# Kernel tuning notes

Measured on AMD Instinct MI355X. Metric: run time of the kernel, lower is better.

The kernel has to match this reference:

```python
import jax, jax.numpy as jnp
import numpy as np

S, H, R, Z, P = 268, 1024, 8, 8, 4
A = S - Z - P          # actual_hidden_dim = 256
E = min(Z, P)          # min_embed_dim = 4
B = 8192


def setup_inputs() -> dict:
    key = jax.random.key(0)
    ks = jax.random.split(key, 16)
    def g(k, shape, scale=0.02):
        return jax.random.normal(k, shape, dtype=jnp.float32) * scale
    return dict(
        t=jax.random.uniform(ks[0], (1,), dtype=jnp.float32) * 24.0,
        state=jax.random.normal(ks[1], (B, S), dtype=jnp.float32),
        W0=g(ks[2], (H, S + 2)), b0=jnp.zeros((H,), jnp.float32),
        res_W1=g(ks[3], (R, H, H)), res_b1=jnp.zeros((R, H), jnp.float32),
        res_W2=g(ks[4], (R, H, H)), res_b2=jnp.zeros((R, H), jnp.float32),
        Wf=g(ks[5], (S, H)), bf=jnp.zeros((S,), jnp.float32),
        lp_in_w=g(ks[6], (3 * E, E)), lp_in_b=jnp.zeros((3 * E,), jnp.float32),
        lp_out_w=g(ks[7], (E, E)), lp_out_b=jnp.zeros((E,), jnp.float32),
        ta_in_w=g(ks[8], (3 * A, A)), ta_in_b=jnp.zeros((3 * A,), jnp.float32),
        ta_out_w=g(ks[9], (A, A)), ta_out_b=jnp.zeros((A,), jnp.float32),
        loc_proj_w=g(ks[10], (E, Z)), loc_proj_b=jnp.zeros((E,), jnp.float32),
        loc_back_w=g(ks[11], (Z, E)), loc_back_b=jnp.zeros((Z,), jnp.float32),
    )


def reference(t, state, W0, b0, res_W1, res_b1, res_W2, res_b2, Wf, bf,
              lp_in_w, lp_in_b, lp_out_w, lp_out_b,
              ta_in_w, ta_in_b, ta_out_w, ta_out_b,
              loc_proj_w, loc_proj_b, loc_back_w, loc_back_b):
    Bn = state.shape[0]
    # time features: [sin(2*pi*t/24), cos(2*pi*t/24)] broadcast to [B, 2]
    ang = t * (2.0 * jnp.pi / 24.0)
    t_vec = jnp.broadcast_to(jnp.concatenate([jnp.sin(ang), jnp.cos(ang)]), (Bn, 2))

    # core MLP trunk: Linear -> ReLU -> R residual blocks -> Linear
    x = jnp.concatenate([state, t_vec], axis=-1)
    h = jax.nn.relu(x @ W0.T + b0)

    def block(h, p):
        W1, b1, W2, b2 = p
        return jnp.tanh(h + jnp.tanh(h @ W1.T + b1) @ W2.T + b2), None

    h, _ = jax.lax.scan(block, h, (res_W1, res_b1, res_W2, res_b2))
    core = h @ Wf.T + bf  # [B, S]

    # Attention deltas. Both MHA calls have key/value seq_len == 1, so the
    # softmax over a single key is exactly 1.0 and the output reduces exactly
    # to out_proj(v_proj(value)); Q/K projections (and the padded time query)
    # cancel mathematically. Same math as nn.MultiheadAttention here.
    h_part = state[:, :A]
    loc = state[:, A:A + Z]
    loc_p = loc @ loc_proj_w.T + loc_proj_b                   # [B, E]
    v = loc_p @ lp_in_w[2 * E:].T + lp_in_b[2 * E:]           # V projection
    enhanced_loc = v @ lp_out_w.T + lp_out_b                  # out projection
    delta_loc = (enhanced_loc - loc_p) @ loc_back_w.T + loc_back_b  # [B, Z]

    v2 = h_part @ ta_in_w[2 * A:].T + ta_in_b[2 * A:]
    enhanced_h = v2 @ ta_out_w.T + ta_out_b
    delta_h = enhanced_h - h_part                             # [B, A]

    delta = jnp.concatenate(
        [delta_h, delta_loc, jnp.zeros((Bn, P), state.dtype)], axis=-1)
    return core + 0.1 * delta
```

## Files before the change

kernel.cpp:

```cpp
#include <hip/hip_runtime.h>
#include <hip/hip_bf16.h>


typedef unsigned short u16;
typedef __bf16 bf16x8 __attribute__((ext_vector_type(8)));
typedef float f32x4 __attribute__((ext_vector_type(4)));

__device__ __forceinline__ u16 f2b(float f) {
  union { float f; unsigned u; } v; v.f = f;
  unsigned r = v.u + 0x7FFFu + ((v.u >> 16) & 1u);
  return (u16)(r >> 16);
}
__device__ __forceinline__ float b2f(u16 s) {
  union { unsigned u; float f; } v; v.u = ((unsigned)s) << 16;
  return v.f;
}

__device__ __forceinline__ void g2l16(const u16* g, u16* l) {
  __builtin_amdgcn_global_load_lds(
      (__attribute__((address_space(1))) void*)g,
      (__attribute__((address_space(3))) void*)l, 16, 0, 0);
}

template<int MODE, int KK, int LDA>
__global__ __launch_bounds__(512, 4)
void pgemm(const u16* __restrict__ A, const u16* __restrict__ W,
           const float* __restrict__ bias, const u16* __restrict__ resid,
           void* __restrict__ outp, int nreal, int ldo)
{
  extern __shared__ __align__(16) u16 sm[];
  constexpr int BUFSZ = (128 + 128) * 64;

  const int tid  = threadIdx.x;
  const int wave = tid >> 6;
  const int lane = tid & 63;
  const int m0 = blockIdx.x << 7;
  const int n0 = blockIdx.y << 7;
  const int wr = wave >> 2, wc = wave & 3;
  const int lrow = lane & 15, quad = lane >> 4;
  const int sw = lrow & 7;

  const int srow  = lane >> 3;
  const int sperm = ((lane & 7) ^ (srow & 7)) << 3;

  const u16* Ag = A + (size_t)(m0 + wave * 16 + srow) * LDA + sperm;
  const u16* Bg = W + (size_t)(n0 + wave * 16 + srow) * KK + sperm;

  f32x4 acc[4][2];
#pragma unroll
  for (int i = 0; i < 4; i++)
#pragma unroll
    for (int j = 0; j < 2; j++) { f32x4 z = {0.f,0.f,0.f,0.f}; acc[i][j] = z; }

  auto stage = [&](int p, int buf) {
    const int ko = p << 6;
    u16* aD = sm + buf * BUFSZ;
    u16* bD = aD + 128 * 64;
    g2l16(Ag + ko,                        aD + (wave * 16 + 0) * 64);
    g2l16(Ag + (size_t)8 * LDA + ko,      aD + (wave * 16 + 8) * 64);
    g2l16(Bg + ko,                        bD + (wave * 16 + 0) * 64);
    g2l16(Bg + (size_t)8 * KK + ko,       bD + (wave * 16 + 8) * 64);
  };

  constexpr int P = KK / 64;

  stage(0, 0);

  for (int p = 0; p < P; ++p) {
    if (p + 1 < P) {
      stage(p + 1, (p + 1) & 1);
      asm volatile("s_waitcnt vmcnt(4)" ::: "memory");
    } else {
      asm volatile("s_waitcnt vmcnt(0)" ::: "memory");
    }
    __builtin_amdgcn_sched_barrier(0);
    __builtin_amdgcn_s_barrier();
    __builtin_amdgcn_sched_barrier(0);

    const u16* aS = sm + (p & 1) * BUFSZ;
    const u16* bS = aS + 128 * 64;
#pragma unroll
    for (int s = 0; s < 2; s++) {
      const int phys = (s * 4 + quad) ^ sw;
      bf16x8 af[4], bfr[2];
#pragma unroll
      for (int i = 0; i < 4; i++)
        af[i] = *(const bf16x8*)&aS[(wr * 64 + i * 16 + lrow) * 64 + phys * 8];
#pragma unroll
      for (int j = 0; j < 2; j++)
        bfr[j] = *(const bf16x8*)&bS[(wc * 32 + j * 16 + lrow) * 64 + phys * 8];
      __builtin_amdgcn_s_setprio(1);
#pragma unroll
      for (int i = 0; i < 4; i++)
#pragma unroll
        for (int j = 0; j < 2; j++)
          acc[i][j] = __builtin_amdgcn_mfma_f32_16x16x32_bf16(af[i], bfr[j], acc[i][j], 0, 0, 0);
      __builtin_amdgcn_s_setprio(0);
    }
    __builtin_amdgcn_sched_barrier(0);
    __builtin_amdgcn_s_barrier();
    __builtin_amdgcn_sched_barrier(0);
  }

  auto th = [](float x) {
    x = fminf(fmaxf(x, -40.f), 40.f);
    float a = __builtin_amdgcn_exp2f(2.88539008177793f * x);
    return (a - 1.f) * __builtin_amdgcn_rcpf(a + 1.f);
  };

#pragma unroll
  for (int i = 0; i < 4; i++) {
    const int rowb = m0 + wr * 64 + i * 16 + quad * 4;
#pragma unroll
    for (int j = 0; j < 2; j++) {
      const int col = n0 + wc * 32 + j * 16 + lrow;
      const float bi = (col < nreal) ? bias[col] : 0.f;
#pragma unroll
      for (int r = 0; r < 4; r++) {
        const int row = rowb + r;
        float v = acc[i][j][r] + bi;
        if (MODE == 0) {
          v = v > 0.f ? v : 0.f;
          ((u16*)outp)[(size_t)row * ldo + col] = f2b(v);
        } else if (MODE == 1) {
          ((u16*)outp)[(size_t)row * ldo + col] = f2b(th(v));
        } else if (MODE == 2) {
          v += b2f(resid[(size_t)row * ldo + col]);
          ((u16*)outp)[(size_t)row * ldo + col] = f2b(th(v));
        } else if (MODE == 3) {
          if (col < nreal) ((float*)outp)[(size_t)row * ldo + col] = v;
        }
      }
    }
  }
}

__global__ __launch_bounds__(256, 4)
void gemm_bt(const u16* __restrict__ A, const u16* __restrict__ B,
             const float* __restrict__ bias, u16* __restrict__ outp,
             int K, int lda, int ldo)
{
  __shared__ __align__(16) u16 As[64 * 64];
  __shared__ __align__(16) u16 Bs[128 * 64];
  const int tid  = threadIdx.x;
  const int wave = tid >> 6;
  const int lane = tid & 63;
  const int m0 = blockIdx.y << 6;
  const int n0 = blockIdx.x << 7;
  const int wr = wave >> 1, wc = wave & 1;
  const int lrow = lane & 15, quad = lane >> 4;
  const int srow  = lane >> 3;
  const int sperm = ((lane & 7) ^ (srow & 7)) << 3;

  const u16* Ag0 = A + (size_t)(m0 + wave * 16 +  0 + srow) * lda + sperm;
  const u16* Ag1 = A + (size_t)(m0 + wave * 16 +  8 + srow) * lda + sperm;
  const u16* Bg0 = B + (size_t)(n0 + wave * 32 +  0 + srow) * K + sperm;
  const u16* Bg1 = B + (size_t)(n0 + wave * 32 +  8 + srow) * K + sperm;
  const u16* Bg2 = B + (size_t)(n0 + wave * 32 + 16 + srow) * K + sperm;
  const u16* Bg3 = B + (size_t)(n0 + wave * 32 + 24 + srow) * K + sperm;
  u16* Al0 = &As[(wave * 16 +  0) * 64];
  u16* Al1 = &As[(wave * 16 +  8) * 64];
  u16* Bl0 = &Bs[(wave * 32 +  0) * 64];
  u16* Bl1 = &Bs[(wave * 32 +  8) * 64];
  u16* Bl2 = &Bs[(wave * 32 + 16) * 64];
  u16* Bl3 = &Bs[(wave * 32 + 24) * 64];

  f32x4 acc[2][4];
#pragma unroll
  for (int i = 0; i < 2; i++)
#pragma unroll
    for (int j = 0; j < 4; j++) { f32x4 z = {0.f,0.f,0.f,0.f}; acc[i][j] = z; }

  const int swz = lrow & 7;

  for (int k0 = 0; k0 < K; k0 += 64) {
    if (k0) __syncthreads();
    g2l16(Ag0 + k0, Al0);
    g2l16(Ag1 + k0, Al1);
    g2l16(Bg0 + k0, Bl0);
    g2l16(Bg1 + k0, Bl1);
    g2l16(Bg2 + k0, Bl2);
    g2l16(Bg3 + k0, Bl3);
    __syncthreads();
#pragma unroll
    for (int s = 0; s < 2; s++) {
      const int c = (s * 4 + quad) ^ swz;
      bf16x8 af[2], bfr[4];
#pragma unroll
      for (int i = 0; i < 2; i++)
        af[i] = *(const bf16x8*)&As[(wr * 32 + i * 16 + lrow) * 64 + c * 8];
#pragma unroll
      for (int j = 0; j < 4; j++)
        bfr[j] = *(const bf16x8*)&Bs[(wc * 64 + j * 16 + lrow) * 64 + c * 8];
#pragma unroll
      for (int i = 0; i < 2; i++)
#pragma unroll
        for (int j = 0; j < 4; j++)
          acc[i][j] = __builtin_amdgcn_mfma_f32_16x16x32_bf16(af[i], bfr[j], acc[i][j], 0, 0, 0);
    }
  }

#pragma unroll
  for (int i = 0; i < 2; i++) {
    const int rowb = m0 + wr * 32 + i * 16 + quad * 4;
#pragma unroll
    for (int j = 0; j < 4; j++) {
      const int col = n0 + wc * 64 + j * 16 + lrow;
      const float bi = bias[col];
#pragma unroll
      for (int r = 0; r < 4; r++)
        outp[(size_t)(rowb + r) * ldo + col] = f2b(acc[i][j][r] + bi);
    }
  }
}

__global__ void conv_bulk(const float* __restrict__ w1, const float* __restrict__ w2,
                          u16* __restrict__ o1, u16* __restrict__ o2)
{
  const int n4 = (8 * 1024 * 1024) / 4;
  int i = blockIdx.x * 256 + threadIdx.x;
  const float* src; u16* dst;
  if (i < n4) { src = w1; dst = o1; }
  else        { i -= n4; if (i >= n4) return; src = w2; dst = o2; }
  float4 v = ((const float4*)src)[i];
  unsigned p0 = (unsigned)f2b(v.x) | ((unsigned)f2b(v.y) << 16);
  unsigned p1 = (unsigned)f2b(v.z) | ((unsigned)f2b(v.w) << 16);
  uint2 pk; pk.x = p0; pk.y = p1;
  ((uint2*)dst)[i] = pk;
}

__global__ void conv_misc(const float* __restrict__ W0, const float* __restrict__ Wf,
                          const float* __restrict__ ta_in_w, const float* __restrict__ ta_out_w,
                          const float* __restrict__ state, const float* __restrict__ t,
                          u16* __restrict__ w0_bf, u16* __restrict__ wf_bf,
                          u16* __restrict__ taA, u16* __restrict__ taB,
                          u16* __restrict__ x_bf)
{
  int i = blockIdx.x * 256 + threadIdx.x;
  const int nW0 = 1024 * 384;
  const int nWf = 384 * 1024;
  const int nTa = 256 * 256;
  const int nX  = 8192 * 384;
  if (i < nW0) {
    int o = i / 384, k = i - o * 384;
    w0_bf[i] = (k < 270) ? f2b(W0[o * 270 + k]) : (u16)0;
    return;
  }
  i -= nW0;
  if (i < nWf) {
    int n = i >> 10;
    wf_bf[i] = (n < 268) ? f2b(Wf[i]) : (u16)0;
    return;
  }
  i -= nWf;
  if (i < nTa) { taA[i] = f2b(ta_in_w[512 * 256 + i]); return; }
  i -= nTa;
  if (i < nTa) { taB[i] = f2b(ta_out_w[i]); return; }
  i -= nTa;
  if (i < nX) {
    int r = i / 384, c = i - r * 384;
    u16 v;
    if (c < 268) v = f2b(state[r * 268 + c]);
    else if (c == 268) { float ang = t[0] * 0.2617993877991494f; v = f2b(sinf(ang)); }
    else if (c == 269) { float ang = t[0] * 0.2617993877991494f; v = f2b(cosf(ang)); }
    else v = 0;
    x_bf[i] = v;
  }
}

__global__ void add_delta(float* __restrict__ out, const u16* __restrict__ eh,
                          const float* __restrict__ state,
                          const float* __restrict__ lp_in_w, const float* __restrict__ lp_in_b,
                          const float* __restrict__ lp_out_w, const float* __restrict__ lp_out_b,
                          const float* __restrict__ loc_proj_w, const float* __restrict__ loc_proj_b,
                          const float* __restrict__ loc_back_w, const float* __restrict__ loc_back_b)
{
  const int idx = blockIdx.x * 256 + threadIdx.x;
  if (idx >= 8192 * 268) return;
  const int row = idx / 268;
  const int col = idx - row * 268;
  if (col < 256) {
    out[idx] += 0.1f * (b2f(eh[row * 256 + col]) - state[idx]);
  } else if (col < 264) {
    const float* srow = state + row * 268 + 256;
    float locp[4], vv[4], dd[4];
#pragma unroll
    for (int e = 0; e < 4; e++) {
      float s = loc_proj_b[e];
#pragma unroll
      for (int z = 0; z < 8; z++) s += loc_proj_w[e * 8 + z] * srow[z];
      locp[e] = s;
    }
#pragma unroll
    for (int e = 0; e < 4; e++) {
      float s = lp_in_b[8 + e];
#pragma unroll
      for (int j = 0; j < 4; j++) s += lp_in_w[(8 + e) * 4 + j] * locp[j];
      vv[e] = s;
    }
#pragma unroll
    for (int e = 0; e < 4; e++) {
      float s = lp_out_b[e];
#pragma unroll
      for (int j = 0; j < 4; j++) s += lp_out_w[e * 4 + j] * vv[j];
      dd[e] = s - locp[e];
    }
    const int z = col - 256;
    float s = loc_back_b[z];
#pragma unroll
    for (int e = 0; e < 4; e++) s += loc_back_w[z * 4 + e] * dd[e];
    out[idx] += 0.1f * s;
  }
}

extern "C" void kernel_launch(void* const* d_in, const int* in_sizes, int n_in,
                              void* d_out, int out_size, void* d_ws, size_t ws_size,
                              hipStream_t stream)
{
  const float* t          = (const float*)d_in[0];
  const float* state      = (const float*)d_in[1];
  const float* W0         = (const float*)d_in[2];
  const float* b0         = (const float*)d_in[3];
  const float* rW1        = (const float*)d_in[4];
  const float* rb1        = (const float*)d_in[5];
  const float* rW2        = (const float*)d_in[6];
  const float* rb2        = (const float*)d_in[7];
  const float* Wf         = (const float*)d_in[8];
  const float* bfv        = (const float*)d_in[9];
  const float* lp_in_w    = (const float*)d_in[10];
  const float* lp_in_b    = (const float*)d_in[11];
  const float* lp_out_w   = (const float*)d_in[12];
  const float* lp_out_b   = (const float*)d_in[13];
  const float* ta_in_w    = (const float*)d_in[14];
  const float* ta_in_b    = (const float*)d_in[15];
  const float* ta_out_w   = (const float*)d_in[16];
  const float* ta_out_b   = (const float*)d_in[17];
  const float* loc_proj_w = (const float*)d_in[18];
  const float* loc_proj_b = (const float*)d_in[19];
  const float* loc_back_w = (const float*)d_in[20];
  const float* loc_back_b = (const float*)d_in[21];
  float* out = (float*)d_out;

  char* ws = (char*)d_ws;
  auto alloc = [&](size_t bytes) { char* p = ws; ws += (bytes + 255) & ~(size_t)255; return p; };
  u16* rw1_bf = (u16*)alloc((size_t)8 * 1024 * 1024 * 2);
  u16* rw2_bf = (u16*)alloc((size_t)8 * 1024 * 1024 * 2);
  u16* w0_bf  = (u16*)alloc((size_t)1024 * 384 * 2);
  u16* wf_bf  = (u16*)alloc((size_t)384 * 1024 * 2);
  u16* taA_bf = (u16*)alloc((size_t)256 * 256 * 2);
  u16* taB_bf = (u16*)alloc((size_t)256 * 256 * 2);
  u16* x_bf   = (u16*)alloc((size_t)8192 * 384 * 2);
  u16* h_bf   = (u16*)alloc((size_t)8192 * 1024 * 2);
  u16* tmp_bf = (u16*)alloc((size_t)8192 * 1024 * 2);
  u16* v2_bf  = (u16*)alloc((size_t)8192 * 256 * 2);
  u16* eh_bf  = (u16*)alloc((size_t)8192 * 256 * 2);

  const int lds = 2 * (128 + 128) * 64 * 2;
  hipFuncSetAttribute(reinterpret_cast<const void*>(pgemm<0, 384, 384>),
                      hipFuncAttributeMaxDynamicSharedMemorySize, lds);
  hipFuncSetAttribute(reinterpret_cast<const void*>(pgemm<1, 1024, 1024>),
                      hipFuncAttributeMaxDynamicSharedMemorySize, lds);
  hipFuncSetAttribute(reinterpret_cast<const void*>(pgemm<2, 1024, 1024>),
                      hipFuncAttributeMaxDynamicSharedMemorySize, lds);
  hipFuncSetAttribute(reinterpret_cast<const void*>(pgemm<3, 1024, 1024>),
                      hipFuncAttributeMaxDynamicSharedMemorySize, lds);

  conv_bulk<<<16384, 256, 0, stream>>>(rW1, rW2, rw1_bf, rw2_bf);
  conv_misc<<<15872, 256, 0, stream>>>(W0, Wf, ta_in_w, ta_out_w, state, t,
                                       w0_bf, wf_bf, taA_bf, taB_bf, x_bf);

  pgemm<0, 384, 384><<<dim3(64, 8), 512, lds, stream>>>(x_bf, w0_bf, b0, nullptr, h_bf, 1024, 1024);

  for (int r = 0; r < 8; r++) {
    pgemm<1, 1024, 1024><<<dim3(64, 8), 512, lds, stream>>>(
        h_bf, rw1_bf + ((size_t)r << 20), rb1 + (r << 10), nullptr, tmp_bf, 1024, 1024);
    pgemm<2, 1024, 1024><<<dim3(64, 8), 512, lds, stream>>>(
        tmp_bf, rw2_bf + ((size_t)r << 20), rb2 + (r << 10), h_bf, h_bf, 1024, 1024);
  }

  gemm_bt<<<dim3(2, 128), 256, 0, stream>>>(x_bf, taA_bf, ta_in_b + 512, v2_bf, 256, 384, 256);
  gemm_bt<<<dim3(2, 128), 256, 0, stream>>>(v2_bf, taB_bf, ta_out_b, eh_bf, 256, 256, 256);

  pgemm<3, 1024, 1024><<<dim3(64, 3), 512, lds, stream>>>(h_bf, wf_bf, bfv, nullptr, out, 268, 268);

  add_delta<<<8576, 256, 0, stream>>>(out, eh_bf, state,
                                      lp_in_w, lp_in_b, lp_out_w, lp_out_b,
                                      loc_proj_w, loc_proj_b, loc_back_w, loc_back_b);
}
```

Measured before the change: 560.3 us.

## Load B tiles directly from global into registers, stage only A in LDS

The weight (B) operand is now loaded by each wave straight from global memory into registers, double-buffered across two register sets, and only the activation (A) tile goes through LDS. This halves LDS use and removes the B LDS reads, which could allow more resident blocks. In exchange, the waves sharing a column slice each issue their own B global loads, relying on L2/L1 for reuse, and register pressure rises. The wait counts are adjusted to cover the extra in-flight loads.

```diff
diff --git a/kernel.cpp b/kernel.cpp
--- a/kernel.cpp
+++ b/kernel.cpp
@@ -29,7 +29,7 @@
            void* __restrict__ outp, int nreal, int ldo)
 {
   extern __shared__ __align__(16) u16 sm[];
-  constexpr int BUFSZ = (128 + 128) * 64;
+  constexpr int BUFSZ = 128 * 64;
 
   const int tid  = threadIdx.x;
   const int wave = tid >> 6;
@@ -44,7 +44,7 @@
   const int sperm = ((lane & 7) ^ (srow & 7)) << 3;
 
   const u16* Ag = A + (size_t)(m0 + wave * 16 + srow) * LDA + sperm;
-  const u16* Bg = W + (size_t)(n0 + wave * 16 + srow) * KK + sperm;
+  const u16* Bg = W + (size_t)(n0 + wc * 32 + lrow) * KK + quad * 8;
 
   f32x4 acc[4][2];
 #pragma unroll
@@ -52,51 +52,68 @@
 #pragma unroll
     for (int j = 0; j < 2; j++) { f32x4 z = {0.f,0.f,0.f,0.f}; acc[i][j] = z; }
 
-  auto stage = [&](int p, int buf) {
+  auto stageA = [&](int p, int buf) {
     const int ko = p << 6;
     u16* aD = sm + buf * BUFSZ;
-    u16* bD = aD + 128 * 64;
-    g2l16(Ag + ko,                        aD + (wave * 16 + 0) * 64);
-    g2l16(Ag + (size_t)8 * LDA + ko,      aD + (wave * 16 + 8) * 64);
-    g2l16(Bg + ko,                        bD + (wave * 16 + 0) * 64);
-    g2l16(Bg + (size_t)8 * KK + ko,       bD + (wave * 16 + 8) * 64);
+    g2l16(Ag + ko,                   aD + (wave * 16 + 0) * 64);
+    g2l16(Ag + (size_t)8 * LDA + ko, aD + (wave * 16 + 8) * 64);
   };
+  auto loadB = [&](int p, bf16x8 (&bb)[2][2]) {
+    const int ko = p << 6;
+#pragma unroll
+    for (int j = 0; j < 2; j++)
+#pragma unroll
+      for (int s = 0; s < 2; s++)
+        bb[j][s] = *(const bf16x8*)(Bg + (size_t)j * 16 * KK + ko + s * 32);
+  };
+  auto compute = [&](const u16* aS, const bf16x8 (&bb)[2][2]) {
+#pragma unroll
+    for (int s = 0; s < 2; s++) {
+      const int phys = (s * 4 + quad) ^ sw;
+      bf16x8 af[4];
+#pragma unroll
+      for (int i = 0; i < 4; i++)
+        af[i] = *(const bf16x8*)&aS[(wr * 64 + i * 16 + lrow) * 64 + phys * 8];
+      __builtin_amdgcn_s_setprio(1);
+#pragma unroll
+      for (int i = 0; i < 4; i++)
+#pragma unroll
+        for (int j = 0; j < 2; j++)
+          acc[i][j] = __builtin_amdgcn_mfma_f32_16x16x32_bf16(af[i], bb[j][s], acc[i][j], 0, 0, 0);
+      __builtin_amdgcn_s_setprio(0);
+    }
+  };
 
   constexpr int P = KK / 64;
-
-  stage(0, 0);
-
-  for (int p = 0; p < P; ++p) {
+  bf16x8 bbA[2][2], bbB[2][2];
+
+  stageA(0, 0); loadB(0, bbA);
+
+  for (int p = 0; p < P; p += 2) {
     if (p + 1 < P) {
-      stage(p + 1, (p + 1) & 1);
-      asm volatile("s_waitcnt vmcnt(4)" ::: "memory");
+      stageA(p + 1, 1); loadB(p + 1, bbB);
+      asm volatile("s_waitcnt vmcnt(6)" ::: "memory");
     } else {
       asm volatile("s_waitcnt vmcnt(0)" ::: "memory");
     }
     __builtin_amdgcn_sched_barrier(0);
     __builtin_amdgcn_s_barrier();
     __builtin_amdgcn_sched_barrier(0);
-
-    const u16* aS = sm + (p & 1) * BUFSZ;
-    const u16* bS = aS + 128 * 64;
-#pragma unroll
-    for (int s = 0; s < 2; s++) {
-      const int phys = (s * 4 + quad) ^ sw;
-      bf16x8 af[4], bfr[2];
-#pragma unroll
-      for (int i = 0; i < 4; i++)
-        af[i] = *(const bf16x8*)&aS[(wr * 64 + i * 16 + lrow) * 64 + phys * 8];
-#pragma unroll
-      for (int j = 0; j < 2; j++)
-        bfr[j] = *(const bf16x8*)&bS[(wc * 32 + j * 16 + lrow) * 64 + phys * 8];
-      __builtin_amdgcn_s_setprio(1);
-#pragma unroll
-      for (int i = 0; i < 4; i++)
-#pragma unroll
-        for (int j = 0; j < 2; j++)
-          acc[i][j] = __builtin_amdgcn_mfma_f32_16x16x32_bf16(af[i], bfr[j], acc[i][j], 0, 0, 0);
-      __builtin_amdgcn_s_setprio(0);
-    }
+    compute(sm, bbA);
+    __builtin_amdgcn_sched_barrier(0);
+    __builtin_amdgcn_s_barrier();
+    __builtin_amdgcn_sched_barrier(0);
+
+    if (p + 2 < P) {
+      stageA(p + 2, 0); loadB(p + 2, bbA);
+      asm volatile("s_waitcnt vmcnt(6)" ::: "memory");
+    } else {
+      asm volatile("s_waitcnt vmcnt(0)" ::: "memory");
+    }
+    __builtin_amdgcn_sched_barrier(0);
+    __builtin_amdgcn_s_barrier();
+    __builtin_amdgcn_sched_barrier(0);
+    compute(sm + BUFSZ, bbB);
     __builtin_amdgcn_sched_barrier(0);
     __builtin_amdgcn_s_barrier();
     __builtin_amdgcn_sched_barrier(0);
@@ -355,7 +372,7 @@
   u16* v2_bf  = (u16*)alloc((size_t)8192 * 256 * 2);
   u16* eh_bf  = (u16*)alloc((size_t)8192 * 256 * 2);
 
-  const int lds = 2 * (128 + 128) * 64 * 2;
+  const int lds = 2 * 128 * 64 * 2;
   hipFuncSetAttribute(reinterpret_cast<const void*>(pgemm<0, 384, 384>),
                       hipFuncAttributeMaxDynamicSharedMemorySize, lds);
   hipFuncSetAttribute(reinterpret_cast<const void*>(pgemm<1, 1024, 1024>),
```

After: 877.8 us. 56.7% more time.

## Fuse the two time-attention projection GEMMs into one kernel via LDS

Applied to the files above, without the earlier changes.

Replaces the two back-to-back gemm_bt launches (V projection, then out projection) with a single kernel. Each block computes a 64-row tile across all 256 output columns, keeps the intermediate v2 tile in padded shared memory, and runs the second GEMM directly from it. This removes one launch and the global write and read of the v2 intermediate. In exchange it uses more shared memory per block (about 74 KB), launches only 128 blocks instead of 256, and gives each wave a larger 4x4 accumulator set, which lowers parallelism.

```diff
diff --git a/kernel.cpp b/kernel.cpp
--- a/kernel.cpp
+++ b/kernel.cpp
@@ -135,83 +135,118 @@
   }
 }
 
-__global__ __launch_bounds__(256, 4)
-void gemm_bt(const u16* __restrict__ A, const u16* __restrict__ B,
-             const float* __restrict__ bias, u16* __restrict__ outp,
-             int K, int lda, int ldo)
-{
-  __shared__ __align__(16) u16 As[64 * 64];
-  __shared__ __align__(16) u16 Bs[128 * 64];
+__global__ __launch_bounds__(256, 2)
+void ta_fused(const u16* __restrict__ x, const u16* __restrict__ taA,
+              const u16* __restrict__ taB,
+              const float* __restrict__ b1, const float* __restrict__ b2,
+              u16* __restrict__ eh)
+{
+  extern __shared__ __align__(16) u16 smf[];
+  u16* As1 = smf;
+  u16* Bs  = smf + 64 * 64;
+  u16* v2L = Bs + 256 * 64;
+
   const int tid  = threadIdx.x;
   const int wave = tid >> 6;
   const int lane = tid & 63;
-  const int m0 = blockIdx.y << 6;
-  const int n0 = blockIdx.x << 7;
-  const int wr = wave >> 1, wc = wave & 1;
+  const int m0 = blockIdx.x << 6;
   const int lrow = lane & 15, quad = lane >> 4;
+  const int sw = lrow & 7;
   const int srow  = lane >> 3;
   const int sperm = ((lane & 7) ^ (srow & 7)) << 3;
 
-  const u16* Ag0 = A + (size_t)(m0 + wave * 16 +  0 + srow) * lda + sperm;
-  const u16* Ag1 = A + (size_t)(m0 + wave * 16 +  8 + srow) * lda + sperm;
-  const u16* Bg0 = B + (size_t)(n0 + wave * 32 +  0 + srow) * K + sperm;
-  const u16* Bg1 = B + (size_t)(n0 + wave * 32 +  8 + srow) * K + sperm;
-  const u16* Bg2 = B + (size_t)(n0 + wave * 32 + 16 + srow) * K + sperm;
-  const u16* Bg3 = B + (size_t)(n0 + wave * 32 + 24 + srow) * K + sperm;
-  u16* Al0 = &As[(wave * 16 +  0) * 64];
-  u16* Al1 = &As[(wave * 16 +  8) * 64];
-  u16* Bl0 = &Bs[(wave * 32 +  0) * 64];
-  u16* Bl1 = &Bs[(wave * 32 +  8) * 64];
-  u16* Bl2 = &Bs[(wave * 32 + 16) * 64];
-  u16* Bl3 = &Bs[(wave * 32 + 24) * 64];
-
-  f32x4 acc[2][4];
-#pragma unroll
-  for (int i = 0; i < 2; i++)
+  const u16* Ag0 = x + (size_t)(m0 + wave * 16 + 0 + srow) * 384 + sperm;
+  const u16* Ag1 = x + (size_t)(m0 + wave * 16 + 8 + srow) * 384 + sperm;
+
+  f32x4 acc[4][4];
+#pragma unroll
+  for (int i = 0; i < 4; i++)
 #pragma unroll
     for (int j = 0; j < 4; j++) { f32x4 z = {0.f,0.f,0.f,0.f}; acc[i][j] = z; }
 
-  const int swz = lrow & 7;
-
-  for (int k0 = 0; k0 < K; k0 += 64) {
+  for (int k0 = 0; k0 < 256; k0 += 64) {
     if (k0) __syncthreads();
-    g2l16(Ag0 + k0, Al0);
-    g2l16(Ag1 + k0, Al1);
-    g2l16(Bg0 + k0, Bl0);
-    g2l16(Bg1 + k0, Bl1);
-    g2l16(Bg2 + k0, Bl2);
-    g2l16(Bg3 + k0, Bl3);
+    g2l16(Ag0 + k0, &As1[(wave * 16 + 0) * 64]);
+    g2l16(Ag1 + k0, &As1[(wave * 16 + 8) * 64]);
+#pragma unroll
+    for (int g = 0; g < 8; g++)
+      g2l16(taA + (size_t)(wave * 64 + g * 8 + srow) * 256 + sperm + k0,
+            &Bs[(wave * 64 + g * 8) * 64]);
     __syncthreads();
 #pragma unroll
     for (int s = 0; s < 2; s++) {
-      const int c = (s * 4 + quad) ^ swz;
-      bf16x8 af[2], bfr[4];
-#pragma unroll
-      for (int i = 0; i < 2; i++)
-        af[i] = *(const bf16x8*)&As[(wr * 32 + i * 16 + lrow) * 64 + c * 8];
+      const int c = (s * 4 + quad) ^ sw;
+      bf16x8 af[4], bfr[4];
+#pragma unroll
+      for (int i = 0; i < 4; i++)
+        af[i] = *(const bf16x8*)&As1[(i * 16 + lrow) * 64 + c * 8];
 #pragma unroll
       for (int j = 0; j < 4; j++)
-        bfr[j] = *(const bf16x8*)&Bs[(wc * 64 + j * 16 + lrow) * 64 + c * 8];
-#pragma unroll
-      for (int i = 0; i < 2; i++)
+        bfr[j] = *(const bf16x8*)&Bs[(wave * 64 + j * 16 + lrow) * 64 + c * 8];
+#pragma unroll
+      for (int i = 0; i < 4; i++)
 #pragma unroll
         for (int j = 0; j < 4; j++)
           acc[i][j] = __builtin_amdgcn_mfma_f32_16x16x32_bf16(af[i], bfr[j], acc[i][j], 0, 0, 0);
     }
   }
-
-#pragma unroll
-  for (int i = 0; i < 2; i++) {
-    const int rowb = m0 + wr * 32 + i * 16 + quad * 4;
+  __syncthreads();
+
+#pragma unroll
+  for (int i = 0; i < 4; i++)
 #pragma unroll
     for (int j = 0; j < 4; j++) {
-      const int col = n0 + wc * 64 + j * 16 + lrow;
-      const float bi = bias[col];
-#pragma unroll
-      for (int r = 0; r < 4; r++)
-        outp[(size_t)(rowb + r) * ldo + col] = f2b(acc[i][j][r] + bi);
-    }
-  }
+      const int col = wave * 64 + j * 16 + lrow;
+      const float bi = b1[col];
+#pragma unroll
+      for (int r = 0; r < 4; r++) {
+        const int row = i * 16 + quad * 4 + r;
+        v2L[row * 264 + col] = f2b(acc[i][j][r] + bi);
+      }
+    }
+#pragma unroll
+  for (int i = 0; i < 4; i++)
+#pragma unroll
+    for (int j = 0; j < 4; j++) { f32x4 z = {0.f,0.f,0.f,0.f}; acc[i][j] = z; }
+  __syncthreads();
+
+  for (int k0 = 0; k0 < 256; k0 += 64) {
+    if (k0) __syncthreads();
+#pragma unroll
+    for (int g = 0; g < 8; g++)
+      g2l16(taB + (size_t)(wave * 64 + g * 8 + srow) * 256 + sperm + k0,
+            &Bs[(wave * 64 + g * 8) * 64]);
+    __syncthreads();
+#pragma unroll
+    for (int s = 0; s < 2; s++) {
+      const int cl = s * 4 + quad;
+      bf16x8 af[4], bfr[4];
+#pragma unroll
+      for (int i = 0; i < 4; i++)
+        af[i] = *(const bf16x8*)&v2L[(i * 16 + lrow) * 264 + k0 + cl * 8];
+#pragma unroll
+      for (int j = 0; j < 4; j++)
+        bfr[j] = *(const bf16x8*)&Bs[(wave * 64 + j * 16 + lrow) * 64 + (cl ^ sw) * 8];
+#pragma unroll
+      for (int i = 0; i < 4; i++)
+#pragma unroll
+        for (int j = 0; j < 4; j++)
+          acc[i][j] = __builtin_amdgcn_mfma_f32_16x16x32_bf16(af[i], bfr[j], acc[i][j], 0, 0, 0);
+    }
+  }
+
+#pragma unroll
+  for (int i = 0; i < 4; i++)
+#pragma unroll
+    for (int j = 0; j < 4; j++) {
+      const int col = wave * 64 + j * 16 + lrow;
+      const float bi = b2[col];
+#pragma unroll
+      for (int r = 0; r < 4; r++) {
+        const int row = m0 + i * 16 + quad * 4 + r;
+        eh[(size_t)row * 256 + col] = f2b(acc[i][j][r] + bi);
+      }
+    }
 }
 
 __global__ void conv_bulk(const float* __restrict__ w1, const float* __restrict__ w2,
@@ -352,7 +387,6 @@
   u16* x_bf   = (u16*)alloc((size_t)8192 * 384 * 2);
   u16* h_bf   = (u16*)alloc((size_t)8192 * 1024 * 2);
   u16* tmp_bf = (u16*)alloc((size_t)8192 * 1024 * 2);
-  u16* v2_bf  = (u16*)alloc((size_t)8192 * 256 * 2);
   u16* eh_bf  = (u16*)alloc((size_t)8192 * 256 * 2);
 
   const int lds = 2 * (128 + 128) * 64 * 2;
@@ -364,6 +398,9 @@
                       hipFuncAttributeMaxDynamicSharedMemorySize, lds);
   hipFuncSetAttribute(reinterpret_cast<const void*>(pgemm<3, 1024, 1024>),
                       hipFuncAttributeMaxDynamicSharedMemorySize, lds);
+  const int ldsT = (64 * 64 + 256 * 64 + 64 * 264) * 2;
+  hipFuncSetAttribute(reinterpret_cast<const void*>(ta_fused),
+                      hipFuncAttributeMaxDynamicSharedMemorySize, ldsT);
 
   conv_bulk<<<16384, 256, 0, stream>>>(rW1, rW2, rw1_bf, rw2_bf);
   conv_misc<<<15872, 256, 0, stream>>>(W0, Wf, ta_in_w, ta_out_w, state, t,
@@ -378,8 +415,8 @@
         tmp_bf, rw2_bf + ((size_t)r << 20), rb2 + (r << 10), h_bf, h_bf, 1024, 1024);
   }
 
-  gemm_bt<<<dim3(2, 128), 256, 0, stream>>>(x_bf, taA_bf, ta_in_b + 512, v2_bf, 256, 384, 256);
-  gemm_bt<<<dim3(2, 128), 256, 0, stream>>>(v2_bf, taB_bf, ta_out_b, eh_bf, 256, 256, 256);
+  ta_fused<<<128, 256, ldsT, stream>>>(x_bf, taA_bf, taB_bf,
+                                       ta_in_b + 512, ta_out_b, eh_bf);
 
   pgemm<3, 1024, 1024><<<dim3(64, 3), 512, lds, stream>>>(h_bf, wf_bf, bfv, nullptr, out, 268, 268);
 
```

New measurement: 566.9 us. No clear change (+1.2%).
